# Performance work log

Measured on AMD Instinct MI355X. Metric: run time of the kernel, lower is better.

Reference implementation:

```python
import jax, jax.numpy as jnp
import numpy as np
import math

B, N, DEG, D, V = 256, 1024, 8, 128, 100000
NN = B * N                     # 262144 nodes
E = NN * DEG                   # 2097152 edges
K1 = math.ceil(0.8 * N)        # 820 kept nodes per graph after pool1
K2 = math.ceil(0.8 * K1)       # 656 after pool2
K3 = math.ceil(0.8 * K2)       # 525 after pool3


def setup_inputs() -> dict:
    key = jax.random.key(0)
    ks = jax.random.split(key, 24)
    x_ids = jax.random.randint(ks[0], (NN, 1), 0, V, dtype=jnp.int32)
    # edges are intra-graph: local endpoints in [0, N) plus per-graph offset
    local = jax.random.randint(ks[1], (2, E), 0, N, dtype=jnp.int32)
    offs = jnp.repeat(jnp.arange(B, dtype=jnp.int32) * N, N * DEG)
    edge_index = local + offs[None, :]
    batch = jnp.repeat(jnp.arange(B, dtype=jnp.int32), N)
    w = lambda k, s: jax.random.normal(k, s, jnp.float32) * 0.05
    inp = dict(x_ids=x_ids, edge_index=edge_index, batch=batch, emb=w(ks[2], (V, D)))
    for i, kk in zip((1, 2, 3), (ks[3:6], ks[6:9], ks[9:12])):
        inp['Wl%d' % i] = w(kk[0], (D, D))
        inp['bl%d' % i] = jnp.zeros((D,), jnp.float32)
        inp['Wr%d' % i] = w(kk[1], (D, D))
        inp['p%d' % i] = w(kk[2], (D,))
    inp['lin1_W'] = w(ks[15], (2 * D, 128)); inp['lin1_b'] = jnp.zeros((128,), jnp.float32)
    inp['lin2_W'] = w(ks[16], (128, 64));    inp['lin2_b'] = jnp.zeros((64,), jnp.float32)
    inp['lin3_W'] = w(ks[17], (64, 1));      inp['lin3_b'] = jnp.zeros((1,), jnp.float32)
    return inp


def _sage(x, src, dst, emask, Wl, bl, Wr):
    # PyG SAGEConv: lin_l(mean_{j in N(i)} x_j) + lin_r(x_i), bias on lin_l
    msg = x[src] * emask[:, None]                                   # [E, D] gather
    agg = jax.ops.segment_sum(msg, dst, num_segments=NN)            # [NN, D] scatter-add
    deg = jax.ops.segment_sum(emask, dst, num_segments=NN)
    agg = agg / jnp.maximum(deg, 1.0)[:, None]
    return agg @ Wl + bl + x @ Wr


def _topk(x, p, nmask, emask, src, dst, k):
    # PyG TopKPooling: score = x.p/||p||; keep top-k per graph; x *= tanh(score)
    score = (x @ p) / jnp.linalg.norm(p)                            # [NN]
    s = jnp.where(nmask, score, -jnp.inf).reshape(B, N)
    order = jnp.argsort(-s, axis=1)
    rank = jnp.argsort(order, axis=1)                               # rank within graph
    keep = (rank < k).reshape(-1) & nmask
    x = jnp.where(keep[:, None], x * jnp.tanh(score)[:, None], 0.0)
    emask = emask * keep[src].astype(emask.dtype) * keep[dst].astype(emask.dtype)
    return x, keep, emask


def _readout(x, nmask, batch):
    # concat(global_max_pool, global_mean_pool) over surviving nodes
    cnt = jax.ops.segment_sum(nmask.astype(x.dtype), batch, num_segments=B)
    mean = jax.ops.segment_sum(x, batch, num_segments=B) / cnt[:, None]
    mx = jax.ops.segment_max(jnp.where(nmask[:, None], x, -jnp.inf), batch, num_segments=B)
    return jnp.concatenate([mx, mean], axis=1)                      # [B, 2D]


def _forward(emb, Wl1, bl1, Wr1, p1, Wl2, bl2, Wr2, p2, Wl3, bl3, Wr3, p3,
             lin1_W, lin1_b, lin2_W, lin2_b, lin3_W, lin3_b,
             x_ids, edge_index, batch):
    src, dst = edge_index[0], edge_index[1]
    x = emb[x_ids[:, 0]]                                            # embedding + squeeze(1)
    nmask = jnp.ones((NN,), bool)
    emask = jnp.ones((E,), jnp.float32)
    x = jax.nn.relu(_sage(x, src, dst, emask, Wl1, bl1, Wr1))
    x, nmask, emask = _topk(x, p1, nmask, emask, src, dst, K1)
    x1 = _readout(x, nmask, batch)
    x = jax.nn.relu(_sage(x, src, dst, emask, Wl2, bl2, Wr2))
    x, nmask, emask = _topk(x, p2, nmask, emask, src, dst, K2)
    x2 = _readout(x, nmask, batch)
    x = jax.nn.relu(_sage(x, src, dst, emask, Wl3, bl3, Wr3))
    x, nmask, emask = _topk(x, p3, nmask, emask, src, dst, K3)
    x3 = _readout(x, nmask, batch)
    h = x1 + x2 + x3                                                # [B, 256]
    h = jax.nn.relu(h @ lin1_W + lin1_b)
    h = jax.nn.relu(h @ lin2_W + lin2_b)                            # dropout is identity at eval
    return jax.nn.sigmoid(h @ lin3_W + lin3_b)[:, 0]                # [B]


def reference(x_ids, edge_index, batch, emb,
              Wl1, bl1, Wr1, p1, Wl2, bl2, Wr2, p2, Wl3, bl3, Wr3, p3,
              lin1_W, lin1_b, lin2_W, lin2_b, lin3_W, lin3_b):
    return _forward(emb, Wl1, bl1, Wr1, p1, Wl2, bl2, Wr2, p2, Wl3, bl3, Wr3, p3,
                    lin1_W, lin1_b, lin2_W, lin2_b, lin3_W, lin3_b,
                    x_ids, edge_index, batch)
```

## Files before the change

kernel.cpp:

```cpp
#include <hip/hip_runtime.h>
#include <math.h>

#define NNODES 262144
#define NEDGE  2097152
#define NB     256
#define NPG    1024
#define EPG    8192
#define DF     128

typedef unsigned short u16;
typedef unsigned int   u32;
typedef __attribute__((ext_vector_type(8))) short  short8;
typedef __attribute__((ext_vector_type(4))) float  floatx4;

static constexpr int K1 = 820, K2 = 656, K3 = 525;

__device__ inline float bflo(u32 u) { union { u32 i; float f; } c; c.i = u << 16;          return c.f; }
__device__ inline float bfhi(u32 u) { union { u32 i; float f; } c; c.i = u & 0xffff0000u;  return c.f; }
__device__ inline u32   f2bf(float f) {
  union { float f; u32 i; } c; c.f = f;
  const u32 r = c.i + 0x7fffu + ((c.i >> 16) & 1u);
  return r >> 16;
}
__device__ inline void acc8(float* b, uint4 v) {
  b[0] += bflo(v.x); b[1] += bfhi(v.x);
  b[2] += bflo(v.y); b[3] += bfhi(v.y);
  b[4] += bflo(v.z); b[5] += bfhi(v.z);
  b[6] += bflo(v.w); b[7] += bfhi(v.w);
}
__device__ inline uint4 pack8(const float* s, float k) {
  uint4 o;
  o.x = f2bf(s[0] * k) | (f2bf(s[1] * k) << 16);
  o.y = f2bf(s[2] * k) | (f2bf(s[3] * k) << 16);
  o.z = f2bf(s[4] * k) | (f2bf(s[5] * k) << 16);
  o.w = f2bf(s[6] * k) | (f2bf(s[7] * k) << 16);
  return o;
}

__global__ __launch_bounds__(1024) void build_csr_k(
    const int* __restrict__ ei, int* __restrict__ csr_src,
    int* __restrict__ row_off, int* __restrict__ row_cnt,
    float* __restrict__ degf, float* __restrict__ keep,
    int* __restrict__ perm)
{
  __shared__ int cnt[NPG];
  __shared__ int roff[NPG];
  __shared__ int wsum[NPG];
  __shared__ int hist[64];
  __shared__ int hoff[64];
  const int b = blockIdx.x, t = threadIdx.x;
  const int* src = ei;
  const int* dst = ei + NEDGE;
  const int e0 = b * EPG;
  cnt[t] = 0;
  __syncthreads();
  for (int e = t; e < EPG; e += 1024) atomicAdd(&cnt[dst[e0 + e] & (NPG - 1)], 1);
  __syncthreads();
  const int v = cnt[t];
  wsum[t] = v;
  __syncthreads();
  for (int off = 1; off < NPG; off <<= 1) {
    const int u = (t >= off) ? wsum[t - off] : 0;
    __syncthreads();
    wsum[t] += u;
    __syncthreads();
  }
  const int base = wsum[t] - v;
  roff[t] = base;
  const int n = b * NPG + t;
  row_off[n] = base;
  row_cnt[n] = v;
  degf[n]    = (float)v;
  keep[n]    = 1.0f;
  if (t < 64) hist[t] = 0;
  __syncthreads();
  for (int e = t; e < EPG; e += 1024) {
    const int dl = dst[e0 + e] & (NPG - 1);
    const int pos = atomicAdd(&roff[dl], 1);
    csr_src[e0 + pos] = src[e0 + e];
  }
  const int bkt = (v < 63) ? v : 63;
  atomicAdd(&hist[bkt], 1);
  __syncthreads();
  if (t == 0) {
    int s = 0;
#pragma unroll 1
    for (int i = 0; i < 64; ++i) { const int h = hist[i]; hoff[i] = s; s += h; }
  }
  __syncthreads();
  const int pp = atomicAdd(&hoff[bkt], 1);
  perm[b * NPG + pp] = t;
}

__global__ __launch_bounds__(256) void gather_k(
    const int* __restrict__ x_ids, const float* __restrict__ emb,
    u16* __restrict__ x0, float* __restrict__ fac)
{
  const int gid = blockIdx.x * 256 + threadIdx.x;
  const int n = gid >> 4, c = gid & 15;
  const int id = x_ids[n];
  const float4 v0 = *(const float4*)(emb + (size_t)id * DF + c * 8);
  const float4 v1 = *(const float4*)(emb + (size_t)id * DF + c * 8 + 4);
  uint4 pk;
  pk.x = f2bf(v0.x) | (f2bf(v0.y) << 16);
  pk.y = f2bf(v0.z) | (f2bf(v0.w) << 16);
  pk.z = f2bf(v1.x) | (f2bf(v1.y) << 16);
  pk.w = f2bf(v1.z) | (f2bf(v1.w) << 16);
  *(uint4*)(x0 + (size_t)n * DF + c * 8) = pk;
  if (c == 0) fac[n] = 1.0f;
}

__global__ __launch_bounds__(64) void wcvt_k(
    const float* __restrict__ Wl1, const float* __restrict__ Wr1,
    const float* __restrict__ Wl2, const float* __restrict__ Wr2,
    const float* __restrict__ Wl3, const float* __restrict__ Wr3,
    u16* __restrict__ wF)
{
  const int f = blockIdx.x & 63, l = blockIdx.x >> 6;
  const int lane = threadIdx.x;
  const int ct = f >> 3, ks = f & 7;
  const int n = ct * 16 + (lane & 15);
  const int k0 = ks * 32 + (lane >> 4) * 8;
  const float* Wl = (l == 0) ? Wl1 : (l == 1) ? Wl2 : Wl3;
  const float* Wr = (l == 0) ? Wr1 : (l == 1) ? Wr2 : Wr3;
  u16 o[8];
#pragma unroll
  for (int j = 0; j < 8; ++j) {
    const int k = k0 + j;
    const float v = (k < 128) ? Wl[k * 128 + n] : Wr[(k - 128) * 128 + n];
    o[j] = (u16)f2bf(v);
  }
  uint4 pk;
  pk.x = (u32)o[0] | ((u32)o[1] << 16);
  pk.y = (u32)o[2] | ((u32)o[3] << 16);
  pk.z = (u32)o[4] | ((u32)o[5] << 16);
  pk.w = (u32)o[6] | ((u32)o[7] << 16);
  *(uint4*)(wF + (((size_t)l * 64 + f) * 64 + lane) * 8) = pk;
}

__global__ __launch_bounds__(1024) void agg_k(
    const u16* __restrict__ xprev, const float* __restrict__ fac,
    const float* __restrict__ keep, const float* __restrict__ deg,
    const int* __restrict__ csr_src, const int* __restrict__ row_off,
    const int* __restrict__ row_cnt, const int* __restrict__ perm,
    u16* __restrict__ aggb, float* __restrict__ ro)
{
  __shared__ u32 xl[16384];
  __shared__ float keepL[NPG];
  __shared__ float4 scr[256];
  const int t = threadIdx.x;
  const int bi = blockIdx.x;
  const int g  = (bi & 7) + 8 * (bi >> 5);
  const int qt = (bi >> 3) & 3;
  const int n  = g * NPG + t;
  {
    const float fr = fac[n];
    const uint4* src = (const uint4*)(xprev + (size_t)n * DF + qt * 32);
    u32* dst = xl + t * 16;
    const int sw = ((t >> 1) & 3) << 2;
#pragma unroll
    for (int j = 0; j < 4; ++j) {
      const uint4 v = src[j];
      uint4 o;
      o.x = f2bf(bflo(v.x) * fr) | (f2bf(bfhi(v.x) * fr) << 16);
      o.y = f2bf(bflo(v.y) * fr) | (f2bf(bfhi(v.y) * fr) << 16);
      o.z = f2bf(bflo(v.z) * fr) | (f2bf(bfhi(v.z) * fr) << 16);
      o.w = f2bf(bflo(v.w) * fr) | (f2bf(bfhi(v.w) * fr) << 16);
      *(uint4*)(dst + ((j << 2) ^ sw)) = o;
    }
    if (ro) keepL[t] = keep[n];
  }
  const int m  = perm[n];
  const int nm = g * NPG + m;
  __syncthreads();
  const int cnt = row_cnt[nm];
  const int* ep = csr_src + g * EPG + row_off[nm];
  float b[32];
#pragma unroll
  for (int j = 0; j < 32; ++j) b[j] = 0.0f;
  int e = 0;
  for (; e + 2 <= cnt; e += 2) {
    const int s0 = ep[e] & (NPG - 1), s1 = ep[e + 1] & (NPG - 1);
    const u32* r0 = xl + s0 * 16; const int w0 = ((s0 >> 1) & 3) << 2;
    const u32* r1 = xl + s1 * 16; const int w1 = ((s1 >> 1) & 3) << 2;
    const uint4 A0 = *(const uint4*)(r0 + (0  ^ w0));
    const uint4 A1 = *(const uint4*)(r0 + (4  ^ w0));
    const uint4 A2 = *(const uint4*)(r0 + (8  ^ w0));
    const uint4 A3 = *(const uint4*)(r0 + (12 ^ w0));
    const uint4 B0 = *(const uint4*)(r1 + (0  ^ w1));
    const uint4 B1 = *(const uint4*)(r1 + (4  ^ w1));
    const uint4 B2 = *(const uint4*)(r1 + (8  ^ w1));
    const uint4 B3 = *(const uint4*)(r1 + (12 ^ w1));
    acc8(b + 0, A0); acc8(b + 8, A1); acc8(b + 16, A2); acc8(b + 24, A3);
    acc8(b + 0, B0); acc8(b + 8, B1); acc8(b + 16, B2); acc8(b + 24, B3);
  }
  if (e < cnt) {
    const int s0 = ep[e] & (NPG - 1);
    const u32* r0 = xl + s0 * 16; const int w0 = ((s0 >> 1) & 3) << 2;
    const uint4 A0 = *(const uint4*)(r0 + (0  ^ w0));
    const uint4 A1 = *(const uint4*)(r0 + (4  ^ w0));
    const uint4 A2 = *(const uint4*)(r0 + (8  ^ w0));
    const uint4 A3 = *(const uint4*)(r0 + (12 ^ w0));
    acc8(b + 0, A0); acc8(b + 8, A1); acc8(b + 16, A2); acc8(b + 24, A3);
  }
  const float inv = 1.0f / fmaxf(deg[nm], 1.0f);
  uint4* op = (uint4*)(aggb + (size_t)nm * DF + qt * 32);
  op[0] = pack8(b + 0,  inv);
  op[1] = pack8(b + 8,  inv);
  op[2] = pack8(b + 16, inv);
  op[3] = pack8(b + 24, inv);
  if (ro) {
    const int dw = t & 15, ck = t >> 4;
    const float NEG = -__builtin_huge_valf();
    float mx0 = NEG, mx1 = NEG, sm0 = 0.0f, sm1 = 0.0f;
#pragma unroll
    for (int i = 0; i < 16; ++i) {
      const int r = ck * 16 + ((i + ck) & 15);
      const u32 u = xl[r * 16 + (dw ^ (((r >> 1) & 3) << 2))];
      if (keepL[r] > 0.5f) {
        const float lo = bflo(u), hi = bfhi(u);
        mx0 = fmaxf(mx0, lo); mx1 = fmaxf(mx1, hi);
        sm0 += lo; sm1 += hi;
      }
    }
    mx0 = fmaxf(mx0, __shfl_xor(mx0, 16, 64));
    mx1 = fmaxf(mx1, __shfl_xor(mx1, 16, 64));
    sm0 += __shfl_xor(sm0, 16, 64);
    sm1 += __shfl_xor(sm1, 16, 64);
    mx0 = fmaxf(mx0, __shfl_xor(mx0, 32, 64));
    mx1 = fmaxf(mx1, __shfl_xor(mx1, 32, 64));
    sm0 += __shfl_xor(sm0, 32, 64);
    sm1 += __shfl_xor(sm1, 32, 64);
    const int lane = t & 63, wv = t >> 6;
    if (lane < 16) scr[wv * 16 + dw] = make_float4(mx0, mx1, sm0, sm1);
    __syncthreads();
    if (t < 16) {
      float4 a = scr[t];
#pragma unroll 1
      for (int w = 1; w < 16; ++w) {
        const float4 c = scr[w * 16 + t];
        a.x = fmaxf(a.x, c.x); a.y = fmaxf(a.y, c.y);
        a.z += c.z; a.w += c.w;
      }
      float* o = ro + (size_t)g * 256;
      o[qt * 32 + 2 * t]           = a.x;
      o[qt * 32 + 2 * t + 1]       = a.y;
      o[128 + qt * 32 + 2 * t]     = a.z;
      o[128 + qt * 32 + 2 * t + 1] = a.w;
    }
  }
}

__global__ __launch_bounds__(512) void gemm_nb_k(
    const u16* __restrict__ G, const u16* __restrict__ F,
    const float* __restrict__ fac,
    const u16* __restrict__ wF, const float* __restrict__ bl,
    const float* __restrict__ p, u16* __restrict__ H,
    float* __restrict__ score)
{
  __shared__ uint4 wL[4096];
  __shared__ float sc[256][2];
  const int t = threadIdx.x;
  const int bi = blockIdx.x;
  const int g   = (bi & 7) + 8 * (bi >> 5);
  const int tpg = (bi >> 3) & 3;
  const int n0  = g * NPG + tpg * 256;
  const int wv = t >> 6, lane = t & 63;
  const int rg = wv >> 1, ch = wv & 1;
  const int lr = lane & 15, quad = lane >> 4;

  {
    const uint4* ws = (const uint4*)wF;
#pragma unroll
    for (int c = 0; c < 8; ++c) wL[t + c * 512] = ws[t + c * 512];
  }
  float4 bn4[4], pn4[4];
#pragma unroll
  for (int ct = 0; ct < 4; ++ct) {
    const int fb = ch * 64 + ct * 16 + quad * 4;
    bn4[ct] = *(const float4*)(bl + fb);
    pn4[ct] = *(const float4*)(p + fb);
  }

  const int rb0 = n0 + rg * 64 + lr;
  short8 agc[4], axc[4], agn[4], axn[4];
  float frc, frn = 0.0f;
#pragma unroll
  for (int ks = 0; ks < 4; ++ks) {
    agn[ks] = (short8)(short)0;
    axn[ks] = (short8)(short)0;
    agc[ks] = *(const short8*)(G + (size_t)rb0 * DF + ks * 32 + quad * 8);
    axc[ks] = *(const short8*)(F + (size_t)rb0 * DF + ks * 32 + quad * 8);
  }
  frc = fac[rb0];
  __syncthreads();

  const short8* wLs = (const short8*)wL;
#pragma unroll
  for (int tl = 0; tl < 4; ++tl) {
    const int row = rb0 + tl * 16;
    if (tl < 3) {
      const int rown = row + 16;
#pragma unroll
      for (int ks = 0; ks < 4; ++ks) {
        agn[ks] = *(const short8*)(G + (size_t)rown * DF + ks * 32 + quad * 8);
        axn[ks] = *(const short8*)(F + (size_t)rown * DF + ks * 32 + quad * 8);
      }
      frn = fac[rown];
    }
    floatx4 aL[4], aR[4];
#pragma unroll
    for (int ct = 0; ct < 4; ++ct) {
      aL[ct] = (floatx4){0.f, 0.f, 0.f, 0.f};
      aR[ct] = (floatx4){0.f, 0.f, 0.f, 0.f};
    }
#pragma unroll
    for (int ks = 0; ks < 4; ++ks)
#pragma unroll
      for (int ct = 0; ct < 4; ++ct) {
        const int f = (ch * 4 + ct) * 8;
        const short8 bfa = wLs[(size_t)(f + ks) * 64 + lane];
        const short8 bfb = wLs[(size_t)(f + ks + 4) * 64 + lane];
        aL[ct] = __builtin_amdgcn_mfma_f32_16x16x32_bf16(bfa, agc[ks], aL[ct], 0, 0, 0);
        aR[ct] = __builtin_amdgcn_mfma_f32_16x16x32_bf16(bfb, axc[ks], aR[ct], 0, 0, 0);
      }
    float si = 0.0f;
#pragma unroll
    for (int ct = 0; ct < 4; ++ct) {
      float v0 = fmaxf(aL[ct][0] + frc * aR[ct][0] + bn4[ct].x, 0.0f);
      float v1 = fmaxf(aL[ct][1] + frc * aR[ct][1] + bn4[ct].y, 0.0f);
      float v2 = fmaxf(aL[ct][2] + frc * aR[ct][2] + bn4[ct].z, 0.0f);
      float v3 = fmaxf(aL[ct][3] + frc * aR[ct][3] + bn4[ct].w, 0.0f);
      si += v0 * pn4[ct].x + v1 * pn4[ct].y + v2 * pn4[ct].z + v3 * pn4[ct].w;
      uint2 st;
      st.x = f2bf(v0) | (f2bf(v1) << 16);
      st.y = f2bf(v2) | (f2bf(v3) << 16);
      *(uint2*)(H + (size_t)row * DF + ch * 64 + ct * 16 + quad * 4) = st;
    }
    si += __shfl_xor(si, 16, 64);
    si += __shfl_xor(si, 32, 64);
    if (lane < 16) sc[rg * 64 + tl * 16 + lr][ch] = si;
#pragma unroll
    for (int ks = 0; ks < 4; ++ks) { agc[ks] = agn[ks]; axc[ks] = axn[ks]; }
    frc = frn;
  }
  __syncthreads();
  if (t < 256) score[n0 + t] = sc[t][0] + sc[t][1];
}

__global__ __launch_bounds__(1024) void rank_k(
    const float* __restrict__ score, const float* __restrict__ p,
    const int* __restrict__ ei,
    float* __restrict__ keep, float* __restrict__ fac,
    float* __restrict__ degN, int K, int next)
{
  __shared__ float s_lds[NPG];
  __shared__ float kfl[NPG];
  __shared__ float deg_l[NPG];
  const int b = blockIdx.x, t = threadIdx.x;
  float ssq = 0.0f;
  for (int d = 0; d < DF; ++d) ssq += p[d] * p[d];
  const float inv_pn = 1.0f / sqrtf(ssq);
  const float NEG = -__builtin_huge_valf();
  {
    const int n = b * NPG + t;
    s_lds[t] = (keep[n] > 0.5f) ? score[n] : NEG;
    deg_l[t] = 0.0f;
  }
  __syncthreads();
  const float si = s_lds[t];
  int rk = 0;
  for (int j = 0; j < NPG; ++j) {
    const float sj = s_lds[j];
    rk += (sj > si) || ((sj == si) && (j < t));
  }
  const bool kp = rk < K;
  const int n = b * NPG + t;
  keep[n] = kp ? 1.0f : 0.0f;
  kfl[t]  = kp ? 1.0f : 0.0f;
  fac[n]  = kp ? tanhf(si * inv_pn) : 0.0f;
  __syncthreads();
  if (next) {
    const int e0 = b * EPG;
    for (int e = t; e < EPG; e += 1024) {
      const int sl = ei[e0 + e] & (NPG - 1);
      const int dl = ei[NEDGE + e0 + e] & (NPG - 1);
      atomicAdd(&deg_l[dl], kfl[sl]);
    }
    __syncthreads();
    degN[n] = deg_l[t];
  }
}

__global__ __launch_bounds__(256) void readout_k(
    const u16* __restrict__ xn, const float* __restrict__ fac,
    const float* __restrict__ keep, float* __restrict__ xlp)
{
  __shared__ float mxA[256], mxB[256], smA[256], smB[256];
  const int blk = blockIdx.x, b = blk >> 3, pr = blk & 7, t = threadIdx.x;
  const int d = t & 63, rq = t >> 6;
  const float NEG = -__builtin_huge_valf();
  float mx0 = NEG, mx1 = NEG, sm0 = 0.0f, sm1 = 0.0f;
  for (int j = 0; j < 32; ++j) {
    const int n = b * NPG + pr * 128 + rq + j * 4;
    const float kf = keep[n];
    const float f  = fac[n];
    const u32 u = *(const u32*)(xn + (size_t)n * DF + d * 2);
    const float v0 = bflo(u) * f, v1 = bfhi(u) * f;
    if (kf > 0.5f) {
      mx0 = fmaxf(mx0, v0); mx1 = fmaxf(mx1, v1);
      sm0 += v0; sm1 += v1;
    }
  }
  mxA[t] = mx0; mxB[t] = mx1; smA[t] = sm0; smB[t] = sm1;
  __syncthreads();
  if (t < 64) {
    float m0 = mxA[t], m1 = mxB[t], s0 = smA[t], s1 = smB[t];
#pragma unroll
    for (int qq = 1; qq < 4; ++qq) {
      m0 = fmaxf(m0, mxA[qq * 64 + t]); m1 = fmaxf(m1, mxB[qq * 64 + t]);
      s0 += smA[qq * 64 + t];           s1 += smB[qq * 64 + t];
    }
    float* o = xlp + (size_t)blk * 256;
    o[2 * t]           = m0;
    o[2 * t + 1]       = m1;
    o[128 + 2 * t]     = s0;
    o[128 + 2 * t + 1] = s1;
  }
}

__global__ __launch_bounds__(256) void mlp_k(
    const float* __restrict__ xlpF, const float* __restrict__ xlp2,
    const float* __restrict__ W1, const float* __restrict__ b1,
    const float* __restrict__ W2, const float* __restrict__ b2,
    const float* __restrict__ W3, const float* __restrict__ b3,
    float* __restrict__ out)
{
  __shared__ float h0[256];
  __shared__ float h1[128];
  __shared__ float h2[64];
  const int b = blockIdx.x, t = threadIdx.x;
  const float invK[3] = {1.0f / (float)K1, 1.0f / (float)K2, 1.0f / (float)K3};
  const float* f0 = xlpF + (size_t)b * 256;
  const float* f1 = xlpF + (size_t)(NB + b) * 256;
  float v;
  if (t < 128) v = f0[t] + f1[t];
  else         v = f0[t] * invK[0] + f1[t] * invK[1];
  {
    const float* base = xlp2 + (size_t)b * 8 * 256;
    if (t < 128) {
      float m = base[t];
#pragma unroll
      for (int pr = 1; pr < 8; ++pr) m = fmaxf(m, base[pr * 256 + t]);
      v += m;
    } else {
      float s = 0.0f;
#pragma unroll
      for (int pr = 0; pr < 8; ++pr) s += base[pr * 256 + t];
      v += s * invK[2];
    }
  }
  h0[t] = v;
  __syncthreads();
  if (t < 128) {
    float a = b1[t];
    for (int k = 0; k < 256; ++k) a += h0[k] * W1[k * 128 + t];
    h1[t] = fmaxf(a, 0.0f);
  }
  __syncthreads();
  if (t < 64) {
    float a = b2[t];
    for (int k = 0; k < 128; ++k) a += h1[k] * W2[k * 64 + t];
    h2[t] = fmaxf(a, 0.0f);
  }
  __syncthreads();
  if (t < 64) {
    float vv = h2[t] * W3[t];
#pragma unroll
    for (int off = 32; off > 0; off >>= 1) vv += __shfl_xor(vv, off, 64);
    if (t == 0) out[b] = 1.0f / (1.0f + expf(-(vv + b3[0])));
  }
}

extern "C" void kernel_launch(void* const* d_in, const int* in_sizes, int n_in,
                              void* d_out, int out_size, void* d_ws, size_t ws_size,
                              hipStream_t stream)
{
  const int*   x_ids = (const int*)d_in[0];
  const int*   ei    = (const int*)d_in[1];
  const float* emb   = (const float*)d_in[3];
  const float* Wl[3]  = {(const float*)d_in[4],  (const float*)d_in[8],  (const float*)d_in[12]};
  const float* blv[3] = {(const float*)d_in[5],  (const float*)d_in[9],  (const float*)d_in[13]};
  const float* Wr[3]  = {(const float*)d_in[6],  (const float*)d_in[10], (const float*)d_in[14]};
  const float* pv[3]  = {(const float*)d_in[7],  (const float*)d_in[11], (const float*)d_in[15]};
  const float* W1 = (const float*)d_in[16]; const float* b1 = (const float*)d_in[17];
  const float* W2 = (const float*)d_in[18]; const float* b2 = (const float*)d_in[19];
  const float* W3 = (const float*)d_in[20]; const float* b3 = (const float*)d_in[21];

  char* ws = (char*)d_ws;
  size_t off = 0;
  auto alloc = [&](size_t bytes) -> void* {
    void* ptr = ws + off; off += (bytes + 255) & ~(size_t)255; return ptr;
  };
  u16*   xA    = (u16*)  alloc((size_t)NNODES * DF * 2);
  u16*   xB    = (u16*)  alloc((size_t)NNODES * DF * 2);
  float* score = (float*)alloc((size_t)NNODES * 4);
  float* keep  = (float*)alloc((size_t)NNODES * 4);
  float* fac   = (float*)alloc((size_t)NNODES * 4);
  float* degf  = (float*)alloc((size_t)NNODES * 4);
  int*   csr   = (int*)  alloc((size_t)NEDGE * 4);
  int*   roff  = (int*)  alloc((size_t)NNODES * 4);
  int*   rcnt  = (int*)  alloc((size_t)NNODES * 4);
  int*   perm  = (int*)  alloc((size_t)NNODES * 4);
  u16*   wF    = (u16*)  alloc((size_t)3 * 64 * 64 * 8 * 2);
  float* xlpF  = (float*)alloc((size_t)2 * NB * 256 * 4);
  float* xlp2  = (float*)alloc((size_t)NB * 8 * 256 * 4);
  const size_t off_base = off;
  u16*   xC    = (u16*)  alloc((size_t)NNODES * DF * 2);
  const bool use3 = (off <= ws_size);
  (void)in_sizes; (void)n_in; (void)out_size;
  if (off_base > ws_size) return;
  if (!use3) return;

  wcvt_k<<<192, 64, 0, stream>>>(Wl[0], Wr[0], Wl[1], Wr[1], Wl[2], Wr[2], wF);
  build_csr_k<<<NB, 1024, 0, stream>>>(ei, csr, roff, rcnt, degf, keep, perm);
  gather_k<<<NNODES * 16 / 256, 256, 0, stream>>>(x_ids, emb, xA, fac);
  const int Ks[3] = {K1, K2, K3};
  u16* F = xA;
  u16* H = xC;
  for (int l = 0; l < 3; ++l) {
    float* ro = (l == 0) ? nullptr : xlpF + (size_t)(l - 1) * NB * 256;
    agg_k<<<1024, 1024, 0, stream>>>(F, fac, keep, degf, csr, roff, rcnt, perm,
                                     xB, ro);
    gemm_nb_k<<<1024, 512, 0, stream>>>(xB, F, fac, wF + (size_t)l * 32768,
                                        blv[l], pv[l], H, score);
    rank_k<<<NB, 1024, 0, stream>>>(score, pv[l], ei, keep, fac, degf,
                                    Ks[l], l < 2 ? 1 : 0);
    u16* tmp = F; F = H; H = tmp;
  }
  readout_k<<<NB * 8, 256, 0, stream>>>(F, fac, keep, xlp2);
  mlp_k<<<NB, 256, 0, stream>>>(xlpF, xlp2, W1, b1, W2, b2, W3, b3, (float*)d_out);
}
```

Measured before the change: 719.9 us.

## Move per-graph readout from agg and separate kernel into rank kernel

The max/mean readout after each pooling stage now runs inside rank_k, right after keep and tanh factors are computed. It reads the new layer output from global memory. Previously this was done inside agg_k of the next layer using LDS-staged data, plus a separate readout_k for the final layer. This removes one kernel launch and the readout work from the aggregation kernel. In exchange, rank_k (only 256 blocks) must read each graph's 1024x128 bf16 features from global memory, which may lengthen that low-parallelism kernel.

```diff
diff --git a/kernel.cpp b/kernel.cpp
--- a/kernel.cpp
+++ b/kernel.cpp
@@ -140,14 +140,12 @@
 
 __global__ __launch_bounds__(1024) void agg_k(
     const u16* __restrict__ xprev, const float* __restrict__ fac,
-    const float* __restrict__ keep, const float* __restrict__ deg,
+    const float* __restrict__ deg,
     const int* __restrict__ csr_src, const int* __restrict__ row_off,
     const int* __restrict__ row_cnt, const int* __restrict__ perm,
-    u16* __restrict__ aggb, float* __restrict__ ro)
+    u16* __restrict__ aggb)
 {
   __shared__ u32 xl[16384];
-  __shared__ float keepL[NPG];
-  __shared__ float4 scr[256];
   const int t = threadIdx.x;
   const int bi = blockIdx.x;
   const int g  = (bi & 7) + 8 * (bi >> 5);
@@ -168,7 +166,6 @@
       o.w = f2bf(bflo(v.w) * fr) | (f2bf(bfhi(v.w) * fr) << 16);
       *(uint4*)(dst + ((j << 2) ^ sw)) = o;
     }
-    if (ro) keepL[t] = keep[n];
   }
   const int m  = perm[n];
   const int nm = g * NPG + m;
@@ -209,46 +206,6 @@
   op[1] = pack8(b + 8,  inv);
   op[2] = pack8(b + 16, inv);
   op[3] = pack8(b + 24, inv);
-  if (ro) {
-    const int dw = t & 15, ck = t >> 4;
-    const float NEG = -__builtin_huge_valf();
-    float mx0 = NEG, mx1 = NEG, sm0 = 0.0f, sm1 = 0.0f;
-#pragma unroll
-    for (int i = 0; i < 16; ++i) {
-      const int r = ck * 16 + ((i + ck) & 15);
-      const u32 u = xl[r * 16 + (dw ^ (((r >> 1) & 3) << 2))];
-      if (keepL[r] > 0.5f) {
-        const float lo = bflo(u), hi = bfhi(u);
-        mx0 = fmaxf(mx0, lo); mx1 = fmaxf(mx1, hi);
-        sm0 += lo; sm1 += hi;
-      }
-    }
-    mx0 = fmaxf(mx0, __shfl_xor(mx0, 16, 64));
-    mx1 = fmaxf(mx1, __shfl_xor(mx1, 16, 64));
-    sm0 += __shfl_xor(sm0, 16, 64);
-    sm1 += __shfl_xor(sm1, 16, 64);
-    mx0 = fmaxf(mx0, __shfl_xor(mx0, 32, 64));
-    mx1 = fmaxf(mx1, __shfl_xor(mx1, 32, 64));
-    sm0 += __shfl_xor(sm0, 32, 64);
-    sm1 += __shfl_xor(sm1, 32, 64);
-    const int lane = t & 63, wv = t >> 6;
-    if (lane < 16) scr[wv * 16 + dw] = make_float4(mx0, mx1, sm0, sm1);
-    __syncthreads();
-    if (t < 16) {
-      float4 a = scr[t];
-#pragma unroll 1
-      for (int w = 1; w < 16; ++w) {
-        const float4 c = scr[w * 16 + t];
-        a.x = fmaxf(a.x, c.x); a.y = fmaxf(a.y, c.y);
-        a.z += c.z; a.w += c.w;
-      }
-      float* o = ro + (size_t)g * 256;
-      o[qt * 32 + 2 * t]           = a.x;
-      o[qt * 32 + 2 * t + 1]       = a.y;
-      o[128 + qt * 32 + 2 * t]     = a.z;
-      o[128 + qt * 32 + 2 * t + 1] = a.w;
-    }
-  }
 }
 
 __global__ __launch_bounds__(512) void gemm_nb_k(
@@ -350,13 +307,15 @@
 
 __global__ __launch_bounds__(1024) void rank_k(
     const float* __restrict__ score, const float* __restrict__ p,
-    const int* __restrict__ ei,
+    const int* __restrict__ ei, const u16* __restrict__ xn,
     float* __restrict__ keep, float* __restrict__ fac,
-    float* __restrict__ degN, int K, int next)
+    float* __restrict__ degN, float* __restrict__ ro, int K, int next)
 {
   __shared__ float s_lds[NPG];
   __shared__ float kfl[NPG];
+  __shared__ float facL[NPG];
   __shared__ float deg_l[NPG];
+  __shared__ float4 red[NPG];
   const int b = blockIdx.x, t = threadIdx.x;
   float ssq = 0.0f;
   for (int d = 0; d < DF; ++d) ssq += p[d] * p[d];
@@ -376,10 +335,29 @@
   }
   const bool kp = rk < K;
   const int n = b * NPG + t;
+  const float fv = kp ? tanhf(si * inv_pn) : 0.0f;
   keep[n] = kp ? 1.0f : 0.0f;
   kfl[t]  = kp ? 1.0f : 0.0f;
-  fac[n]  = kp ? tanhf(si * inv_pn) : 0.0f;
-  __syncthreads();
+  facL[t] = fv;
+  fac[n]  = fv;
+  __syncthreads();
+  {
+    const int dw = t & 63, rq = t >> 6;
+    float mx0 = NEG, mx1 = NEG, sm0 = 0.0f, sm1 = 0.0f;
+    const u16* xrow = xn + ((size_t)b * NPG + (size_t)rq * 64) * DF;
+#pragma unroll 4
+    for (int j = 0; j < 64; ++j) {
+      const int r = rq * 64 + j;
+      if (kfl[r] > 0.5f) {
+        const u32 u = *(const u32*)(xrow + (size_t)j * DF + dw * 2);
+        const float f = facL[r];
+        const float v0 = bflo(u) * f, v1 = bfhi(u) * f;
+        mx0 = fmaxf(mx0, v0); mx1 = fmaxf(mx1, v1);
+        sm0 += v0; sm1 += v1;
+      }
+    }
+    red[t] = make_float4(mx0, mx1, sm0, sm1);
+  }
   if (next) {
     const int e0 = b * EPG;
     for (int e = t; e < EPG; e += 1024) {
@@ -387,50 +365,27 @@
       const int dl = ei[NEDGE + e0 + e] & (NPG - 1);
       atomicAdd(&deg_l[dl], kfl[sl]);
     }
-    __syncthreads();
-    degN[n] = deg_l[t];
-  }
-}
-
-__global__ __launch_bounds__(256) void readout_k(
-    const u16* __restrict__ xn, const float* __restrict__ fac,
-    const float* __restrict__ keep, float* __restrict__ xlp)
-{
-  __shared__ float mxA[256], mxB[256], smA[256], smB[256];
-  const int blk = blockIdx.x, b = blk >> 3, pr = blk & 7, t = threadIdx.x;
-  const int d = t & 63, rq = t >> 6;
-  const float NEG = -__builtin_huge_valf();
-  float mx0 = NEG, mx1 = NEG, sm0 = 0.0f, sm1 = 0.0f;
-  for (int j = 0; j < 32; ++j) {
-    const int n = b * NPG + pr * 128 + rq + j * 4;
-    const float kf = keep[n];
-    const float f  = fac[n];
-    const u32 u = *(const u32*)(xn + (size_t)n * DF + d * 2);
-    const float v0 = bflo(u) * f, v1 = bfhi(u) * f;
-    if (kf > 0.5f) {
-      mx0 = fmaxf(mx0, v0); mx1 = fmaxf(mx1, v1);
-      sm0 += v0; sm1 += v1;
-    }
-  }
-  mxA[t] = mx0; mxB[t] = mx1; smA[t] = sm0; smB[t] = sm1;
-  __syncthreads();
+  }
+  __syncthreads();
+  if (next) degN[n] = deg_l[t];
   if (t < 64) {
-    float m0 = mxA[t], m1 = mxB[t], s0 = smA[t], s1 = smB[t];
-#pragma unroll
-    for (int qq = 1; qq < 4; ++qq) {
-      m0 = fmaxf(m0, mxA[qq * 64 + t]); m1 = fmaxf(m1, mxB[qq * 64 + t]);
-      s0 += smA[qq * 64 + t];           s1 += smB[qq * 64 + t];
-    }
-    float* o = xlp + (size_t)blk * 256;
-    o[2 * t]           = m0;
-    o[2 * t + 1]       = m1;
-    o[128 + 2 * t]     = s0;
-    o[128 + 2 * t + 1] = s1;
+    float4 a = red[t];
+#pragma unroll 1
+    for (int w = 1; w < 16; ++w) {
+      const float4 c = red[w * 64 + t];
+      a.x = fmaxf(a.x, c.x); a.y = fmaxf(a.y, c.y);
+      a.z += c.z; a.w += c.w;
+    }
+    float* o = ro + (size_t)b * 256;
+    o[2 * t]           = a.x;
+    o[2 * t + 1]       = a.y;
+    o[128 + 2 * t]     = a.z;
+    o[128 + 2 * t + 1] = a.w;
   }
 }
 
 __global__ __launch_bounds__(256) void mlp_k(
-    const float* __restrict__ xlpF, const float* __restrict__ xlp2,
+    const float* __restrict__ xlpF,
     const float* __restrict__ W1, const float* __restrict__ b1,
     const float* __restrict__ W2, const float* __restrict__ b2,
     const float* __restrict__ W3, const float* __restrict__ b3,
@@ -443,23 +398,10 @@
   const float invK[3] = {1.0f / (float)K1, 1.0f / (float)K2, 1.0f / (float)K3};
   const float* f0 = xlpF + (size_t)b * 256;
   const float* f1 = xlpF + (size_t)(NB + b) * 256;
+  const float* f2 = xlpF + (size_t)(2 * NB + b) * 256;
   float v;
-  if (t < 128) v = f0[t] + f1[t];
-  else         v = f0[t] * invK[0] + f1[t] * invK[1];
-  {
-    const float* base = xlp2 + (size_t)b * 8 * 256;
-    if (t < 128) {
-      float m = base[t];
-#pragma unroll
-      for (int pr = 1; pr < 8; ++pr) m = fmaxf(m, base[pr * 256 + t]);
-      v += m;
-    } else {
-      float s = 0.0f;
-#pragma unroll
-      for (int pr = 0; pr < 8; ++pr) s += base[pr * 256 + t];
-      v += s * invK[2];
-    }
-  }
+  if (t < 128) v = f0[t] + f1[t] + f2[t];
+  else         v = f0[t] * invK[0] + f1[t] * invK[1] + f2[t] * invK[2];
   h0[t] = v;
   __syncthreads();
   if (t < 128) {
@@ -513,8 +455,7 @@
   int*   rcnt  = (int*)  alloc((size_t)NNODES * 4);
   int*   perm  = (int*)  alloc((size_t)NNODES * 4);
   u16*   wF    = (u16*)  alloc((size_t)3 * 64 * 64 * 8 * 2);
-  float* xlpF  = (float*)alloc((size_t)2 * NB * 256 * 4);
-  float* xlp2  = (float*)alloc((size_t)NB * 8 * 256 * 4);
+  float* xlpF  = (float*)alloc((size_t)3 * NB * 256 * 4);
   const size_t off_base = off;
   u16*   xC    = (u16*)  alloc((size_t)NNODES * DF * 2);
   const bool use3 = (off <= ws_size);
@@ -529,15 +470,13 @@
   u16* F = xA;
   u16* H = xC;
   for (int l = 0; l < 3; ++l) {
-    float* ro = (l == 0) ? nullptr : xlpF + (size_t)(l - 1) * NB * 256;
-    agg_k<<<1024, 1024, 0, stream>>>(F, fac, keep, degf, csr, roff, rcnt, perm,
-                                     xB, ro);
+    agg_k<<<1024, 1024, 0, stream>>>(F, fac, degf, csr, roff, rcnt, perm, xB);
     gemm_nb_k<<<1024, 512, 0, stream>>>(xB, F, fac, wF + (size_t)l * 32768,
                                         blv[l], pv[l], H, score);
-    rank_k<<<NB, 1024, 0, stream>>>(score, pv[l], ei, keep, fac, degf,
+    rank_k<<<NB, 1024, 0, stream>>>(score, pv[l], ei, H, keep, fac, degf,
+                                    xlpF + (size_t)l * NB * 256,
                                     Ks[l], l < 2 ? 1 : 0);
     u16* tmp = F; F = H; H = tmp;
   }
-  readout_k<<<NB * 8, 256, 0, stream>>>(F, fac, keep, xlp2);
-  mlp_k<<<NB, 256, 0, stream>>>(xlpF, xlp2, W1, b1, W2, b2, W3, b3, (float*)d_out);
-}
+  mlp_k<<<NB, 256, 0, stream>>>(xlpF, W1, b1, W2, b2, W3, b3, (float*)d_out);
+}
```

Result: no change. 731.0 us (+1.5%).

## Replace O(N^2) rank counting with radix-select top-k and separate readout kernel

Applied to the files above, without the earlier changes.

The per-graph top-k in rank_k used to compare every node against all 1024 others. It now uses a 4-pass, 8-bit radix select over order-preserving score keys, with LDS histograms, and resolves ties by node index using ballot and prefix counts. The fused readout in agg_k (max and sum over kept nodes) is removed, and readout_k now runs after every layer, so agg_k is smaller but there are three readout launches instead of one. The radix passes add several block barriers and a serial 256-bin scan on one thread in exchange for removing the quadratic compare loop.

```diff
diff --git a/kernel.cpp b/kernel.cpp
--- a/kernel.cpp
+++ b/kernel.cpp
@@ -10,6 +10,7 @@
 
 typedef unsigned short u16;
 typedef unsigned int   u32;
+typedef unsigned long long u64;
 typedef __attribute__((ext_vector_type(8))) short  short8;
 typedef __attribute__((ext_vector_type(4))) float  floatx4;
 
@@ -140,14 +141,12 @@
 
 __global__ __launch_bounds__(1024) void agg_k(
     const u16* __restrict__ xprev, const float* __restrict__ fac,
-    const float* __restrict__ keep, const float* __restrict__ deg,
+    const float* __restrict__ deg,
     const int* __restrict__ csr_src, const int* __restrict__ row_off,
     const int* __restrict__ row_cnt, const int* __restrict__ perm,
-    u16* __restrict__ aggb, float* __restrict__ ro)
+    u16* __restrict__ aggb)
 {
   __shared__ u32 xl[16384];
-  __shared__ float keepL[NPG];
-  __shared__ float4 scr[256];
   const int t = threadIdx.x;
   const int bi = blockIdx.x;
   const int g  = (bi & 7) + 8 * (bi >> 5);
@@ -168,7 +167,6 @@
       o.w = f2bf(bflo(v.w) * fr) | (f2bf(bfhi(v.w) * fr) << 16);
       *(uint4*)(dst + ((j << 2) ^ sw)) = o;
     }
-    if (ro) keepL[t] = keep[n];
   }
   const int m  = perm[n];
   const int nm = g * NPG + m;
@@ -209,46 +207,6 @@
   op[1] = pack8(b + 8,  inv);
   op[2] = pack8(b + 16, inv);
   op[3] = pack8(b + 24, inv);
-  if (ro) {
-    const int dw = t & 15, ck = t >> 4;
-    const float NEG = -__builtin_huge_valf();
-    float mx0 = NEG, mx1 = NEG, sm0 = 0.0f, sm1 = 0.0f;
-#pragma unroll
-    for (int i = 0; i < 16; ++i) {
-      const int r = ck * 16 + ((i + ck) & 15);
-      const u32 u = xl[r * 16 + (dw ^ (((r >> 1) & 3) << 2))];
-      if (keepL[r] > 0.5f) {
-        const float lo = bflo(u), hi = bfhi(u);
-        mx0 = fmaxf(mx0, lo); mx1 = fmaxf(mx1, hi);
-        sm0 += lo; sm1 += hi;
-      }
-    }
-    mx0 = fmaxf(mx0, __shfl_xor(mx0, 16, 64));
-    mx1 = fmaxf(mx1, __shfl_xor(mx1, 16, 64));
-    sm0 += __shfl_xor(sm0, 16, 64);
-    sm1 += __shfl_xor(sm1, 16, 64);
-    mx0 = fmaxf(mx0, __shfl_xor(mx0, 32, 64));
-    mx1 = fmaxf(mx1, __shfl_xor(mx1, 32, 64));
-    sm0 += __shfl_xor(sm0, 32, 64);
-    sm1 += __shfl_xor(sm1, 32, 64);
-    const int lane = t & 63, wv = t >> 6;
-    if (lane < 16) scr[wv * 16 + dw] = make_float4(mx0, mx1, sm0, sm1);
-    __syncthreads();
-    if (t < 16) {
-      float4 a = scr[t];
-#pragma unroll 1
-      for (int w = 1; w < 16; ++w) {
-        const float4 c = scr[w * 16 + t];
-        a.x = fmaxf(a.x, c.x); a.y = fmaxf(a.y, c.y);
-        a.z += c.z; a.w += c.w;
-      }
-      float* o = ro + (size_t)g * 256;
-      o[qt * 32 + 2 * t]           = a.x;
-      o[qt * 32 + 2 * t + 1]       = a.y;
-      o[128 + qt * 32 + 2 * t]     = a.z;
-      o[128 + qt * 32 + 2 * t + 1] = a.w;
-    }
-  }
 }
 
 __global__ __launch_bounds__(512) void gemm_nb_k(
@@ -354,31 +312,63 @@
     float* __restrict__ keep, float* __restrict__ fac,
     float* __restrict__ degN, int K, int next)
 {
-  __shared__ float s_lds[NPG];
+  __shared__ int hist[256];
+  __shared__ int hsel[2];
+  __shared__ int wtie[16];
   __shared__ float kfl[NPG];
   __shared__ float deg_l[NPG];
   const int b = blockIdx.x, t = threadIdx.x;
   float ssq = 0.0f;
   for (int d = 0; d < DF; ++d) ssq += p[d] * p[d];
   const float inv_pn = 1.0f / sqrtf(ssq);
-  const float NEG = -__builtin_huge_valf();
+  const int n = b * NPG + t;
+  const float sc = score[n];
+  const bool act = keep[n] > 0.5f;
+  u32 u;
   {
-    const int n = b * NPG + t;
-    s_lds[t] = (keep[n] > 0.5f) ? score[n] : NEG;
-    deg_l[t] = 0.0f;
-  }
-  __syncthreads();
-  const float si = s_lds[t];
-  int rk = 0;
-  for (int j = 0; j < NPG; ++j) {
-    const float sj = s_lds[j];
-    rk += (sj > si) || ((sj == si) && (j < t));
-  }
-  const bool kp = rk < K;
-  const int n = b * NPG + t;
+    union { float f; u32 i; } c; c.f = sc;
+    u = (c.i & 0x80000000u) ? ~c.i : (c.i | 0x80000000u);
+    if (!act) u = 0u;
+  }
+  deg_l[t] = 0.0f;
+  u32 prefix = 0, pmask = 0;
+  int Kr = K;
+#pragma unroll 1
+  for (int pass = 0; pass < 4; ++pass) {
+    const int shift = 24 - pass * 8;
+    if (t < 256) hist[t] = 0;
+    __syncthreads();
+    if ((u & pmask) == prefix) atomicAdd(&hist[(u >> shift) & 255], 1);
+    __syncthreads();
+    if (t == 0) {
+      int c = 0, bsel = 0;
+#pragma unroll 1
+      for (int bb = 255; bb >= 0; --bb) {
+        const int h = hist[bb];
+        if (c + h >= Kr) { bsel = bb; break; }
+        c += h;
+      }
+      hsel[0] = bsel; hsel[1] = c;
+    }
+    __syncthreads();
+    prefix |= ((u32)hsel[0]) << shift;
+    pmask  |= 0xFFu << shift;
+    Kr     -= hsel[1];
+  }
+  const int lane = t & 63, wv = t >> 6;
+  const bool tie = (u == prefix);
+  const u64 mb = __ballot(tie);
+  const int tl = __popcll(mb & ((1ULL << lane) - 1ULL));
+  if (lane == 0) wtie[wv] = (int)__popcll(mb);
+  __syncthreads();
+  int tsum = 0;
+#pragma unroll
+  for (int w = 0; w < 16; ++w) tsum += (w < wv) ? wtie[w] : 0;
+  const bool kp = (u > prefix) || (tie && (tsum + tl) < Kr);
+  const float fv = kp ? tanhf(sc * inv_pn) : 0.0f;
   keep[n] = kp ? 1.0f : 0.0f;
+  fac[n]  = fv;
   kfl[t]  = kp ? 1.0f : 0.0f;
-  fac[n]  = kp ? tanhf(si * inv_pn) : 0.0f;
   __syncthreads();
   if (next) {
     const int e0 = b * EPG;
@@ -430,7 +420,7 @@
 }
 
 __global__ __launch_bounds__(256) void mlp_k(
-    const float* __restrict__ xlpF, const float* __restrict__ xlp2,
+    const float* __restrict__ xlp,
     const float* __restrict__ W1, const float* __restrict__ b1,
     const float* __restrict__ W2, const float* __restrict__ b2,
     const float* __restrict__ W3, const float* __restrict__ b3,
@@ -441,13 +431,10 @@
   __shared__ float h2[64];
   const int b = blockIdx.x, t = threadIdx.x;
   const float invK[3] = {1.0f / (float)K1, 1.0f / (float)K2, 1.0f / (float)K3};
-  const float* f0 = xlpF + (size_t)b * 256;
-  const float* f1 = xlpF + (size_t)(NB + b) * 256;
-  float v;
-  if (t < 128) v = f0[t] + f1[t];
-  else         v = f0[t] * invK[0] + f1[t] * invK[1];
-  {
-    const float* base = xlp2 + (size_t)b * 8 * 256;
+  float v = 0.0f;
+#pragma unroll
+  for (int l = 0; l < 3; ++l) {
+    const float* base = xlp + ((size_t)l * NB * 8 + (size_t)b * 8) * 256;
     if (t < 128) {
       float m = base[t];
 #pragma unroll
@@ -457,7 +444,7 @@
       float s = 0.0f;
 #pragma unroll
       for (int pr = 0; pr < 8; ++pr) s += base[pr * 256 + t];
-      v += s * invK[2];
+      v += s * invK[l];
     }
   }
   h0[t] = v;
@@ -513,8 +500,7 @@
   int*   rcnt  = (int*)  alloc((size_t)NNODES * 4);
   int*   perm  = (int*)  alloc((size_t)NNODES * 4);
   u16*   wF    = (u16*)  alloc((size_t)3 * 64 * 64 * 8 * 2);
-  float* xlpF  = (float*)alloc((size_t)2 * NB * 256 * 4);
-  float* xlp2  = (float*)alloc((size_t)NB * 8 * 256 * 4);
+  float* xlp   = (float*)alloc((size_t)3 * NB * 8 * 256 * 4);
   const size_t off_base = off;
   u16*   xC    = (u16*)  alloc((size_t)NNODES * DF * 2);
   const bool use3 = (off <= ws_size);
@@ -529,15 +515,14 @@
   u16* F = xA;
   u16* H = xC;
   for (int l = 0; l < 3; ++l) {
-    float* ro = (l == 0) ? nullptr : xlpF + (size_t)(l - 1) * NB * 256;
-    agg_k<<<1024, 1024, 0, stream>>>(F, fac, keep, degf, csr, roff, rcnt, perm,
-                                     xB, ro);
+    agg_k<<<1024, 1024, 0, stream>>>(F, fac, degf, csr, roff, rcnt, perm, xB);
     gemm_nb_k<<<1024, 512, 0, stream>>>(xB, F, fac, wF + (size_t)l * 32768,
                                         blv[l], pv[l], H, score);
     rank_k<<<NB, 1024, 0, stream>>>(score, pv[l], ei, keep, fac, degf,
                                     Ks[l], l < 2 ? 1 : 0);
+    readout_k<<<NB * 8, 256, 0, stream>>>(H, fac, keep,
+                                          xlp + (size_t)l * NB * 8 * 256);
     u16* tmp = F; F = H; H = tmp;
   }
-  readout_k<<<NB * 8, 256, 0, stream>>>(F, fac, keep, xlp2);
-  mlp_k<<<NB, 256, 0, stream>>>(xlpF, xlp2, W1, b1, W2, b2, W3, b3, (float*)d_out);
-}
+  mlp_k<<<NB, 256, 0, stream>>>(xlp, W1, b1, W2, b2, W3, b3, (float*)d_out);
+}
```

Result: slower. 802.9 us (+11.5%).
